# Optimization experiments

Measured on AMD Instinct MI355X. Metric: run time of the kernel, lower is better.

Reference implementation:

```python
import jax, jax.numpy as jnp
import numpy as np
from jax import lax

PATCH_SIZE = 7
NEIGH_SIZE = 9
SIGMA = 2.0
EPS = 1e-05


def _gaussian_kernel(sigma, sz):
    mid = sz // 2
    ax = np.arange(sz) - mid
    g = np.exp(-(ax[:, None] ** 2 + ax[None, :] ** 2) / (2.0 * sigma ** 2)) / (2.0 * np.pi * sigma ** 2)
    return g.astype(np.float32)


KERNEL = jnp.asarray(_gaussian_kernel(SIGMA, PATCH_SIZE))[None, None]  # (1,1,7,7)

_half = NEIGH_SIZE // 2
SHIFTS = jnp.asarray(
    [(x, y) for x in range(-_half, NEIGH_SIZE - _half)
     for y in range(-_half, NEIGH_SIZE - _half) if (x, y) != (0, 0)],
    dtype=jnp.int32)  # (80, 2) — xshift outer loop, yshift inner, matching torch order
SHIFTS4 = jnp.asarray([(-1, 0), (1, 0), (0, -1), (0, 1)], dtype=jnp.int32)


def _translate(img, tx, ty):
    # Faithful to torch affine_grid + grid_sample(nearest, zeros, align_corners=False):
    # a 'translation' of tx in normalized coords samples input at pixel j + tx*W/2.
    # H, W even and tx, ty integers -> exact integer pixel shifts, zero padding.
    H, W = img.shape
    px = jnp.arange(W) + tx * (W // 2)
    py = jnp.arange(H) + ty * (H // 2)
    mask = ((py >= 0) & (py < H))[:, None] & ((px >= 0) & (px < W))[None, :]
    out = img[jnp.clip(py, 0, H - 1)[:, None], jnp.clip(px, 0, W - 1)[None, :]]
    return jnp.where(mask, out, jnp.zeros((), img.dtype))


def _blur(x):
    # x: (N, H, W); conv2d with gaussian kernel, stride 1, padding 3 (same for 7x7)
    y = lax.conv_general_dilated(x[:, None], KERNEL, (1, 1), [(3, 3), (3, 3)],
                                 dimension_numbers=('NCHW', 'OIHW', 'NCHW'))
    return y[:, 0]


def _dp_batch(img2d, shifts):
    # Dp for a batch of shifts: shift, diff, square, gaussian blur
    shifted = jax.vmap(lambda s: _translate(img2d, s[0], s[1]))(shifts)  # (N,H,W)
    return _blur((img2d[None] - shifted) ** 2)


def setup_inputs() -> dict:
    key = jax.random.key(0)
    k1, k2 = jax.random.split(key)
    image1 = jax.random.normal(k1, (1, 1, 1024, 1024), dtype=jnp.float32)
    image2 = jax.random.normal(k2, (1, 1, 1024, 1024), dtype=jnp.float32)
    return {"image1": image1, "image2": image2}


def reference(image1, image2):
    img1 = image1[0, 0]  # (H, W)
    img2 = image2[0, 0]
    H, W = img1.shape
    reduce_size = (PATCH_SIZE + NEIGH_SIZE - 2) // 2  # = 7
    # Vimg: average of 4 single-pixel-neighborhood Dp's on image1, + eps
    Vimg = _dp_batch(img1, SHIFTS4).sum(axis=0) / 4.0 + EPS  # (H, W)
    # 80-shift MIND responses on image2
    D2 = _dp_batch(img2, SHIFTS)  # (80, H, W)
    mind = jnp.exp(-D2 / Vimg[None])
    # torch slices: dim1 end index is (C - reduce_size) = 1-7 = -6 -> H-6;
    # dim2 end index is (H - reduce_size). Replicated exactly (H == W).
    out = mind[:, reduce_size:H + 1 - reduce_size, reduce_size:H - reduce_size]
    mx = jnp.max(out, axis=0)
    return jnp.mean(out / mx[None])
```

## Files before the change

kernel.cpp:

```cpp
#include <hip/hip_runtime.h>
#include <cmath>

#define IMG_W 1024
#define SROWS 22
#define SCOLS 70

struct GK { float gh[7]; float gv[7]; };

__device__ __forceinline__ float warp_block_sum(float v, float* wsum, int tx, int ty) {
    #pragma unroll
    for (int off = 32; off > 0; off >>= 1)
        v += __shfl_down(v, off, 64);
    if (tx == 0) wsum[ty] = v;
    __syncthreads();
    return wsum[0] + wsum[1] + wsum[2] + wsum[3];
}

__global__ __launch_bounds__(256)
void mind_tile(const float* __restrict__ img1, const float* __restrict__ img2,
               float* __restrict__ partials, GK gk)
{
    __shared__ float4 s1[SROWS * SCOLS];

    const int tx  = (int)threadIdx.x;
    const int ty  = (int)threadIdx.y;
    const int tid = ty * 64 + tx;
    const int x0  = 7 + 64 * (int)blockIdx.x;
    const int y0  = 7 + 16 * (int)blockIdx.y;

    #pragma unroll
    for (int k = 0; k < 7; ++k) {
        const int e = tid + 256 * k;
        if (e < SROWS * SCOLS) {
            const int r  = e / SCOLS;
            const int c  = e - r * SCOLS;
            const int sr = min(y0 - 3 + r, 1023);
            const int sc = min(x0 - 3 + c, 1023);
            const int srp = sr ^ 512;
            const int scp = sc ^ 512;
            const float a  = img2[sr  * IMG_W + sc ];
            const float b  = img2[sr  * IMG_W + scp];
            const float cc = img2[srp * IMG_W + sc ];
            const float d  = img2[srp * IMG_W + scp];
            const float u  = img1[sr  * IMG_W + sc ];
            const float ub = img1[sr  * IMG_W + scp];
            const float uc = img1[srp * IMG_W + sc ];
            const float a2 = a * a;
            const float tb = a - b, tc = a - cc, td = a - d;
            const float su = u - ub, sv = u - uc;
            float4 f;
            f.x = fmaf(tb, tb, -a2);
            f.y = fmaf(tc, tc, -a2);
            f.z = fmaf(td, td, -a2);
            f.w = fmaf(u, u + u, fmaf(su, su, sv * sv));
            s1[e] = f;
        }
    }
    __syncthreads();

    const bool xs = (x0 - 3 <= 511) && (x0 + 66 >= 512);
    const bool ys = (y0 - 3 <= 511) && (y0 + 18 >= 512);
    const bool xok = (x0 + tx <= 1016);
    float tsum = 0.f;

    if (!xs && !ys) {
        const bool xlo = ((x0 & 512) == 0);
        const bool ylo = ((y0 & 512) == 0);
        float Px[4] = {0,0,0,0}, Py[4] = {0,0,0,0}, Pd[4] = {0,0,0,0}, V4[4] = {0,0,0,0};
        #pragma unroll
        for (int r = 0; r < 10; ++r) {
            const float4* __restrict__ row = &s1[(4 * ty + r) * SCOLS + tx];
            float hH = 0, hV = 0, hD = 0, hU = 0;
            #pragma unroll
            for (int kx = 0; kx < 7; ++kx) {
                const float4 g = row[kx];
                hH = fmaf(gk.gh[kx], g.x, hH);
                hV = fmaf(gk.gh[kx], g.y, hV);
                hD = fmaf(gk.gh[kx], g.z, hD);
                hU = fmaf(gk.gh[kx], g.w, hU);
            }
            #pragma unroll
            for (int o = 0; o < 4; ++o) {
                if (r - o >= 0 && r - o <= 6) {
                    const float g = gk.gv[r - o];
                    Px[o] = fmaf(g, hH, Px[o]);
                    Py[o] = fmaf(g, hV, Py[o]);
                    Pd[o] = fmaf(g, hD, Pd[o]);
                    V4[o] = fmaf(g, hU, V4[o]);
                }
            }
        }
        (void)xlo; (void)ylo;
        #pragma unroll
        for (int o = 0; o < 4; ++o) {
            const float V = fmaf(V4[o], 0.25f, 1e-5f);
            const float invV = 1.0f / V;
            float M = fminf(0.f, Px[o]);
            M = fminf(M, Py[o]); M = fminf(M, Pd[o]);
            const float pix = 77.f * __expf(M * invV)
                + __expf((M - Px[o]) * invV)
                + __expf((M - Py[o]) * invV)
                + __expf((M - Pd[o]) * invV);
            const bool ok = xok && (y0 + 4 * ty + o <= 1017);
            tsum += ok ? pix : 0.f;
        }
    } else {
        float glx[7], ghx[7];
        #pragma unroll
        for (int kx = 0; kx < 7; ++kx) {
            const bool lo = (((x0 - 3 + tx + kx) & 512) == 0);
            glx[kx] = lo ? gk.gh[kx] : 0.f;
            ghx[kx] = lo ? 0.f : gk.gh[kx];
        }
        float Ph[4]  = {0,0,0,0}, Qh[4]  = {0,0,0,0}, Pv[4] = {0,0,0,0}, Qv[4] = {0,0,0,0};
        float Ppp[4] = {0,0,0,0}, Ppm[4] = {0,0,0,0}, Pmp[4] = {0,0,0,0}, Pmm[4] = {0,0,0,0};
        float V4[4]  = {0,0,0,0};
        #pragma unroll
        for (int r = 0; r < 10; ++r) {
            const float4* __restrict__ row = &s1[(4 * ty + r) * SCOLS + tx];
            float hHlo = 0, hHhi = 0, hV = 0, hDlo = 0, hDhi = 0, hU = 0;
            #pragma unroll
            for (int kx = 0; kx < 7; ++kx) {
                const float4 g = row[kx];
                hHlo = fmaf(glx[kx],   g.x, hHlo);
                hHhi = fmaf(ghx[kx],   g.x, hHhi);
                hV   = fmaf(gk.gh[kx], g.y, hV);
                hDlo = fmaf(glx[kx],   g.z, hDlo);
                hDhi = fmaf(ghx[kx],   g.z, hDhi);
                hU   = fmaf(gk.gh[kx], g.w, hU);
            }
            const bool ylo = (((y0 + 4 * ty - 3 + r) & 512) == 0);
            #pragma unroll
            for (int o = 0; o < 4; ++o) {
                if (r - o >= 0 && r - o <= 6) {
                    const float g  = gk.gv[r - o];
                    const float wl = ylo ? g : 0.f;
                    const float wh = ylo ? 0.f : g;
                    Ph [o] = fmaf(g,  hHlo, Ph [o]);
                    Qh [o] = fmaf(g,  hHhi, Qh [o]);
                    Pv [o] = fmaf(wl, hV,   Pv [o]);
                    Qv [o] = fmaf(wh, hV,   Qv [o]);
                    Ppp[o] = fmaf(wl, hDlo, Ppp[o]);
                    Ppm[o] = fmaf(wh, hDlo, Ppm[o]);
                    Pmp[o] = fmaf(wl, hDhi, Pmp[o]);
                    Pmm[o] = fmaf(wh, hDhi, Pmm[o]);
                    V4 [o] = fmaf(g,  hU,   V4 [o]);
                }
            }
        }
        #pragma unroll
        for (int o = 0; o < 4; ++o) {
            const float V = fmaf(V4[o], 0.25f, 1e-5f);
            const float invV = 1.0f / V;
            float M = fminf(0.f, Ph[o]);
            M = fminf(M, Qh[o]);  M = fminf(M, Pv[o]);  M = fminf(M, Qv[o]);
            M = fminf(M, Ppp[o]); M = fminf(M, Pmp[o]); M = fminf(M, Ppm[o]); M = fminf(M, Pmm[o]);
            const float pix = 72.f * __expf(M * invV)
                + __expf((M - Ph [o]) * invV) + __expf((M - Qh [o]) * invV)
                + __expf((M - Pv [o]) * invV) + __expf((M - Qv [o]) * invV)
                + __expf((M - Ppp[o]) * invV) + __expf((M - Pmp[o]) * invV)
                + __expf((M - Ppm[o]) * invV) + __expf((M - Pmm[o]) * invV);
            const bool ok = xok && (y0 + 4 * ty + o <= 1017);
            tsum += ok ? pix : 0.f;
        }
    }

    __shared__ float wsum[4];
    const float bt = warp_block_sum(tsum, wsum, tx, ty);
    if (tid == 0)
        partials[(int)blockIdx.y * gridDim.x + (int)blockIdx.x] = bt;
}

__global__ __launch_bounds__(256)
void mind_reduce(const float* __restrict__ partials, float* __restrict__ out)
{
    float s = 0.f;
    #pragma unroll
    for (int k = 0; k < 4; ++k)
        s += partials[(int)threadIdx.x + 256 * k];
    double d = (double)s;
    #pragma unroll
    for (int off = 32; off > 0; off >>= 1)
        d += __shfl_down(d, off, 64);
    __shared__ double sm[4];
    const int lane = (int)threadIdx.x & 63, wid = (int)threadIdx.x >> 6;
    if (lane == 0) sm[wid] = d;
    __syncthreads();
    if (threadIdx.x == 0)
        out[0] = (float)((sm[0] + sm[1] + sm[2] + sm[3]) / 81688800.0);
}

extern "C" void kernel_launch(void* const* d_in, const int* in_sizes, int n_in,
                              void* d_out, int out_size, void* d_ws, size_t ws_size,
                              hipStream_t stream) {
    const float* img1 = (const float*)d_in[0];
    const float* img2 = (const float*)d_in[1];
    float* out = (float*)d_out;
    float* partials = (float*)d_ws;

    GK gk;
    for (int i = 0; i < 7; ++i) {
        const double d = i - 3;
        gk.gh[i] = (float)std::exp(-(d * d) / 8.0);
        gk.gv[i] = (float)(std::exp(-(d * d) / 8.0) / (8.0 * M_PI));
    }

    dim3 block(64, 4);
    dim3 grid(16, 64);
    mind_tile<<<grid, block, 0, stream>>>(img1, img2, partials, gk);
    mind_reduce<<<1, 256, 0, stream>>>(partials, out);
}
```

Measured before the change: 70.77 us.

## Share horizontal blur rows via LDS and fuse final reduction with atomics

In the interior path, the horizontal 7-tap pass is now computed once per staged row and written to a second shared buffer, so threads no longer recompute overlapping horizontal sums for each of their output rows. The separate reduce kernel is replaced by atomic accumulation into 64 strided slots plus a last-block-done counter that writes the final mean. This removes redundant FMAs and one kernel launch, but adds an extra barrier and more LDS per block, an atomic tail, and a memset of the workspace. The sum is now accumulated in float rather than double.

Measured after the change: 86.16 us. 1.22x slower.

```diff
diff --git a/kernel.cpp b/kernel.cpp
--- a/kernel.cpp
+++ b/kernel.cpp
@@ -4,23 +4,19 @@
 #define IMG_W 1024
 #define SROWS 22
 #define SCOLS 70
+#define NBLOCKS 1024
+#define NSLOTS 64
 
 struct GK { float gh[7]; float gv[7]; };
-
-__device__ __forceinline__ float warp_block_sum(float v, float* wsum, int tx, int ty) {
-    #pragma unroll
-    for (int off = 32; off > 0; off >>= 1)
-        v += __shfl_down(v, off, 64);
-    if (tx == 0) wsum[ty] = v;
-    __syncthreads();
-    return wsum[0] + wsum[1] + wsum[2] + wsum[3];
-}
 
 __global__ __launch_bounds__(256)
 void mind_tile(const float* __restrict__ img1, const float* __restrict__ img2,
-               float* __restrict__ partials, GK gk)
+               float* __restrict__ ws, float* __restrict__ out, GK gk)
 {
     __shared__ float4 s1[SROWS * SCOLS];
+    __shared__ float4 s2[SROWS * 64];
+    __shared__ float  wsum[4];
+    __shared__ int    lastflag;
 
     const int tx  = (int)threadIdx.x;
     const int ty  = (int)threadIdx.y;
@@ -64,33 +60,40 @@
     float tsum = 0.f;
 
     if (!xs && !ys) {
-        const bool xlo = ((x0 & 512) == 0);
-        const bool ylo = ((y0 & 512) == 0);
+        #pragma unroll
+        for (int j = 0; j < 6; ++j) {
+            const int r = ty + 4 * j;
+            if (r < SROWS) {
+                const float4* __restrict__ row = &s1[r * SCOLS + tx];
+                float4 h = make_float4(0.f, 0.f, 0.f, 0.f);
+                #pragma unroll
+                for (int kx = 0; kx < 7; ++kx) {
+                    const float4 g = row[kx];
+                    h.x = fmaf(gk.gh[kx], g.x, h.x);
+                    h.y = fmaf(gk.gh[kx], g.y, h.y);
+                    h.z = fmaf(gk.gh[kx], g.z, h.z);
+                    h.w = fmaf(gk.gh[kx], g.w, h.w);
+                }
+                s2[r * 64 + tx] = h;
+            }
+        }
+        __syncthreads();
+
         float Px[4] = {0,0,0,0}, Py[4] = {0,0,0,0}, Pd[4] = {0,0,0,0}, V4[4] = {0,0,0,0};
         #pragma unroll
         for (int r = 0; r < 10; ++r) {
-            const float4* __restrict__ row = &s1[(4 * ty + r) * SCOLS + tx];
-            float hH = 0, hV = 0, hD = 0, hU = 0;
-            #pragma unroll
-            for (int kx = 0; kx < 7; ++kx) {
-                const float4 g = row[kx];
-                hH = fmaf(gk.gh[kx], g.x, hH);
-                hV = fmaf(gk.gh[kx], g.y, hV);
-                hD = fmaf(gk.gh[kx], g.z, hD);
-                hU = fmaf(gk.gh[kx], g.w, hU);
-            }
+            const float4 h = s2[(4 * ty + r) * 64 + tx];
             #pragma unroll
             for (int o = 0; o < 4; ++o) {
                 if (r - o >= 0 && r - o <= 6) {
                     const float g = gk.gv[r - o];
-                    Px[o] = fmaf(g, hH, Px[o]);
-                    Py[o] = fmaf(g, hV, Py[o]);
-                    Pd[o] = fmaf(g, hD, Pd[o]);
-                    V4[o] = fmaf(g, hU, V4[o]);
+                    Px[o] = fmaf(g, h.x, Px[o]);
+                    Py[o] = fmaf(g, h.y, Py[o]);
+                    Pd[o] = fmaf(g, h.z, Pd[o]);
+                    V4[o] = fmaf(g, h.w, V4[o]);
                 }
             }
         }
-        (void)xlo; (void)ylo;
         #pragma unroll
         for (int o = 0; o < 4; ++o) {
             const float V = fmaf(V4[o], 0.25f, 1e-5f);
@@ -165,29 +168,30 @@
         }
     }
 
-    __shared__ float wsum[4];
-    const float bt = warp_block_sum(tsum, wsum, tx, ty);
-    if (tid == 0)
-        partials[(int)blockIdx.y * gridDim.x + (int)blockIdx.x] = bt;
-}
-
-__global__ __launch_bounds__(256)
-void mind_reduce(const float* __restrict__ partials, float* __restrict__ out)
-{
-    float s = 0.f;
-    #pragma unroll
-    for (int k = 0; k < 4; ++k)
-        s += partials[(int)threadIdx.x + 256 * k];
-    double d = (double)s;
     #pragma unroll
     for (int off = 32; off > 0; off >>= 1)
-        d += __shfl_down(d, off, 64);
-    __shared__ double sm[4];
-    const int lane = (int)threadIdx.x & 63, wid = (int)threadIdx.x >> 6;
-    if (lane == 0) sm[wid] = d;
+        tsum += __shfl_down(tsum, off, 64);
+    if (tx == 0) wsum[ty] = tsum;
     __syncthreads();
-    if (threadIdx.x == 0)
-        out[0] = (float)((sm[0] + sm[1] + sm[2] + sm[3]) / 81688800.0);
+
+    if (tid == 0) {
+        const float bt = wsum[0] + wsum[1] + wsum[2] + wsum[3];
+        const int bid = (int)blockIdx.y * gridDim.x + (int)blockIdx.x;
+        atomicAdd(&ws[(bid & (NSLOTS - 1)) * 16], bt);
+        __threadfence();
+        const unsigned t = atomicAdd((unsigned*)(ws + 1024), 1u);
+        lastflag = (t == NBLOCKS - 1) ? 1 : 0;
+    }
+    __syncthreads();
+    if (lastflag && ty == 0) {
+        __threadfence();
+        float v = atomicAdd(&ws[tx * 16], 0.0f);
+        #pragma unroll
+        for (int off = 32; off > 0; off >>= 1)
+            v += __shfl_down(v, off, 64);
+        if (tx == 0)
+            out[0] = v * (1.0f / 81688800.0f);
+    }
 }
 
 extern "C" void kernel_launch(void* const* d_in, const int* in_sizes, int n_in,
@@ -196,7 +200,7 @@
     const float* img1 = (const float*)d_in[0];
     const float* img2 = (const float*)d_in[1];
     float* out = (float*)d_out;
-    float* partials = (float*)d_ws;
+    float* ws = (float*)d_ws;
 
     GK gk;
     for (int i = 0; i < 7; ++i) {
@@ -205,8 +209,8 @@
         gk.gv[i] = (float)(std::exp(-(d * d) / 8.0) / (8.0 * M_PI));
     }
 
+    hipMemsetAsync(d_ws, 0, (1024 + 1) * sizeof(float), stream);
     dim3 block(64, 4);
     dim3 grid(16, 64);
-    mind_tile<<<grid, block, 0, stream>>>(img1, img2, partials, gk);
-    mind_reduce<<<1, 256, 0, stream>>>(partials, out);
+    mind_tile<<<grid, block, 0, stream>>>(img1, img2, ws, out, gk);
 }
```
